# Kernel optimization log

Hardware: AMD Instinct MI355X
Metric: run time of the kernel (lower is better)

Reference implementation:

```python
import jax, jax.numpy as jnp
import numpy as np

B, NQ, NK, DQ, DK, H, DV = 4, 128, 1024, 256, 256, 256, 256
MASK_VAL = -1e6


def setup_inputs() -> dict:
    key = jax.random.key(0)
    ks = jax.random.split(key, 7)
    queries = jax.random.normal(ks[0], (B, NQ, DQ), dtype=jnp.float32)
    keys = jax.random.normal(ks[1], (B, NK, DK), dtype=jnp.float32)
    values = jax.random.normal(ks[2], (B, NK, DV), dtype=jnp.float32)
    # per-batch valid lengths in [1, NK]
    valid_lens = jax.random.randint(ks[3], (B,), 1, NK + 1, dtype=jnp.int64 if jax.config.read('jax_enable_x64') else jnp.int32)
    W_q = jax.random.normal(ks[4], (DQ, H), dtype=jnp.float32) * (1.0 / np.sqrt(DQ))
    W_k = jax.random.normal(ks[5], (DK, H), dtype=jnp.float32) * (1.0 / np.sqrt(DK))
    v_w = jax.random.normal(ks[6], (H,), dtype=jnp.float32) * (1.0 / np.sqrt(H))
    return {"queries": queries, "keys": keys, "values": values,
            "valid_lens": valid_lens, "W_q": W_q, "W_k": W_k, "v_w": v_w}


def reference(queries, keys, values, valid_lens, W_q, W_k, v_w):
    # Project queries and keys to the shared hidden space.
    q = jnp.einsum('bqd,dh->bqh', queries, W_q)          # (B, NQ, H)
    k = jnp.einsum('bkd,dh->bkh', keys, W_k)             # (B, NK, H)
    # Broadcast-add + tanh -> (B, NQ, NK, H), then contract with v to scores.
    features = jnp.tanh(q[:, :, None, :] + k[:, None, :, :])
    scores = jnp.einsum('bqkh,h->bqk', features, v_w)    # (B, NQ, NK)
    # Masked softmax over the key axis: positions >= valid_len get -1e6.
    nk = scores.shape[-1]
    mask = jnp.arange(nk)[None, None, :] < valid_lens[:, None, None]
    scores = jnp.where(mask, scores, MASK_VAL)
    attention_weights = jax.nn.softmax(scores, axis=-1)
    # Weighted sum of values (bmm).
    return jnp.einsum('bqk,bkv->bqv', attention_weights, values)
```

## Files before the change

### kernel.cpp

```cpp
#include <hip/hip_runtime.h>

#define B_   4
#define NQ_  128
#define NK_  1024
#define DD_  256
#define H_   256
#define DV_  256
#define QB   2

__device__ __forceinline__ float wave_sum(float v) {
  #pragma unroll
  for (int o = 32; o; o >>= 1) v += __shfl_xor(v, o);
  return v;
}
__device__ __forceinline__ float wave_max(float v) {
  #pragma unroll
  for (int o = 32; o; o >>= 1) v = fmaxf(v, __shfl_xor(v, o));
  return v;
}

template <bool TRANS>
__global__ __launch_bounds__(256) void proj_kernel(const float* __restrict__ A,
                                                   const float* __restrict__ W,
                                                   float* __restrict__ C) {
  __shared__ float As[16 * 68];
  __shared__ float Ws[16 * 68];
  const int tid  = threadIdx.x;
  const int row0 = blockIdx.x * 64;
  const int col0 = blockIdx.y * 64;
  const int ld_d = tid & 15, ld_r = tid >> 4;
  const int lw_n = tid & 63, lw_k = tid >> 6;
  const int tn = tid & 15, tm = tid >> 4;
  float acc[4][4] = {};
  for (int kt = 0; kt < DD_ / 16; ++kt) {
    const int k0 = kt * 16;
    #pragma unroll
    for (int p = 0; p < 4; ++p) {
      const int r = p * 16 + ld_r;
      As[ld_d * 68 + r] = A[(size_t)(row0 + r) * DD_ + (k0 + ld_d)];
    }
    #pragma unroll
    for (int p = 0; p < 4; ++p) {
      const int kk = p * 4 + lw_k;
      Ws[kk * 68 + lw_n] = W[(size_t)(k0 + kk) * H_ + (col0 + lw_n)];
    }
    __syncthreads();
    #pragma unroll
    for (int kk = 0; kk < 16; ++kk) {
      const float4 a = *(const float4*)&As[kk * 68 + tm * 4];
      const float4 w = *(const float4*)&Ws[kk * 68 + tn * 4];
      acc[0][0] = fmaf(a.x, w.x, acc[0][0]);
      acc[0][1] = fmaf(a.x, w.y, acc[0][1]);
      acc[0][2] = fmaf(a.x, w.z, acc[0][2]);
      acc[0][3] = fmaf(a.x, w.w, acc[0][3]);
      acc[1][0] = fmaf(a.y, w.x, acc[1][0]);
      acc[1][1] = fmaf(a.y, w.y, acc[1][1]);
      acc[1][2] = fmaf(a.y, w.z, acc[1][2]);
      acc[1][3] = fmaf(a.y, w.w, acc[1][3]);
      acc[2][0] = fmaf(a.z, w.x, acc[2][0]);
      acc[2][1] = fmaf(a.z, w.y, acc[2][1]);
      acc[2][2] = fmaf(a.z, w.z, acc[2][2]);
      acc[2][3] = fmaf(a.z, w.w, acc[2][3]);
      acc[3][0] = fmaf(a.w, w.x, acc[3][0]);
      acc[3][1] = fmaf(a.w, w.y, acc[3][1]);
      acc[3][2] = fmaf(a.w, w.z, acc[3][2]);
      acc[3][3] = fmaf(a.w, w.w, acc[3][3]);
    }
    __syncthreads();
  }
  if (!TRANS) {
    #pragma unroll
    for (int i = 0; i < 4; ++i) {
      float4 v = make_float4(acc[i][0], acc[i][1], acc[i][2], acc[i][3]);
      *(float4*)&C[(size_t)(row0 + tm * 4 + i) * H_ + (col0 + tn * 4)] = v;
    }
  } else {
    #pragma unroll
    for (int i = 0; i < 4; ++i) {
      const int row = row0 + tm * 4 + i;
      const int b = row >> 10;
      const int k = row & (NK_ - 1);
      #pragma unroll
      for (int j = 0; j < 4; ++j) {
        const int h = col0 + tn * 4 + j;
        C[((size_t)(b * H_ + h)) * NK_ + k] = acc[i][j];
      }
    }
  }
}

__global__ __launch_bounds__(512) void fused_attn_kernel(const float* __restrict__ qp,
                                                         const float* __restrict__ kpT,
                                                         const float* __restrict__ v_w,
                                                         const float* __restrict__ values,
                                                         const int* __restrict__ valid_lens,
                                                         float* __restrict__ out) {
  __shared__ float qs[QB][H_];
  __shared__ float w2s[H_];
  __shared__ float reds[4];
  __shared__ float s_lds[QB][NK_];
  __shared__ float redm[QB][4];
  __shared__ float redsum[QB][4];
  __shared__ float red[8][QB][DV_];

  const int tid = threadIdx.x;
  const int n = blockIdx.x;
  const int xcd = n & 7;
  const int b = xcd >> 1;
  const int idx = ((n >> 3) << 1) | (xcd & 1);

  int vl = valid_lens[b];
  vl = vl < 1 ? 1 : (vl > NK_ ? NK_ : vl);

  if (tid < H_) {
    const float vw = v_w[tid];
    w2s[tid] = 2.0f * vw;
    float s = wave_sum(vw);
    if ((tid & 63) == 0) reds[tid >> 6] = s;
  }
  {
    const int qi = tid >> 8, h = tid & 255;
    qs[qi][h] = qp[(size_t)(b * NQ_ + idx * QB + qi) * H_ + h];
  }
  __syncthreads();
  const float wsum = reds[0] + reds[1] + reds[2] + reds[3];

  const int k0 = tid * 2;
  const float C2 = 2.8853900817779268f;
  if (k0 < vl) {
    float a00 = 0.f, a01 = 0.f, a10 = 0.f, a11 = 0.f;
    const float* kp = kpT + (size_t)b * H_ * NK_ + k0;
    #pragma unroll 4
    for (int h = 0; h < H_; ++h) {
      const float2 kv = *(const float2*)(kp + (size_t)h * NK_);
      const float w2 = w2s[h];
      const float q0 = qs[0][h];
      const float q1 = qs[1][h];
      const float e00 = __builtin_amdgcn_exp2f((q0 + kv.x) * C2);
      const float e01 = __builtin_amdgcn_exp2f((q0 + kv.y) * C2);
      const float e10 = __builtin_amdgcn_exp2f((q1 + kv.x) * C2);
      const float e11 = __builtin_amdgcn_exp2f((q1 + kv.y) * C2);
      a00 = fmaf(w2, __builtin_amdgcn_rcpf(1.0f + e00), a00);
      a01 = fmaf(w2, __builtin_amdgcn_rcpf(1.0f + e01), a01);
      a10 = fmaf(w2, __builtin_amdgcn_rcpf(1.0f + e10), a10);
      a11 = fmaf(w2, __builtin_amdgcn_rcpf(1.0f + e11), a11);
    }
    *(float2*)&s_lds[0][k0] = make_float2(wsum - a00, wsum - a01);
    *(float2*)&s_lds[1][k0] = make_float2(wsum - a10, wsum - a11);
  }
  __syncthreads();

  const int qi = tid >> 8;
  const int kk0 = (tid & 255) * 4;
  const float4 s4 = *(const float4*)&s_lds[qi][kk0];
  const float NEG = -3.0e38f;
  float m = NEG;
  m = fmaxf(m, (kk0 + 0 < vl) ? s4.x : NEG);
  m = fmaxf(m, (kk0 + 1 < vl) ? s4.y : NEG);
  m = fmaxf(m, (kk0 + 2 < vl) ? s4.z : NEG);
  m = fmaxf(m, (kk0 + 3 < vl) ? s4.w : NEG);
  m = wave_max(m);
  if ((tid & 63) == 0) redm[qi][(tid >> 6) & 3] = m;
  __syncthreads();
  const float M = fmaxf(fmaxf(redm[qi][0], redm[qi][1]), fmaxf(redm[qi][2], redm[qi][3]));
  const float CE = 1.4426950408889634f;
  const float p0 = (kk0 + 0 < vl) ? __builtin_amdgcn_exp2f((s4.x - M) * CE) : 0.0f;
  const float p1 = (kk0 + 1 < vl) ? __builtin_amdgcn_exp2f((s4.y - M) * CE) : 0.0f;
  const float p2 = (kk0 + 2 < vl) ? __builtin_amdgcn_exp2f((s4.z - M) * CE) : 0.0f;
  const float p3 = (kk0 + 3 < vl) ? __builtin_amdgcn_exp2f((s4.w - M) * CE) : 0.0f;
  float psum = wave_sum(p0 + p1 + p2 + p3);
  if ((tid & 63) == 0) redsum[qi][(tid >> 6) & 3] = psum;
  __syncthreads();
  const float S = redsum[qi][0] + redsum[qi][1] + redsum[qi][2] + redsum[qi][3];
  const float inv = 1.0f / S;
  *(float4*)&s_lds[qi][kk0] = make_float4(p0 * inv, p1 * inv, p2 * inv, p3 * inv);
  __syncthreads();

  const int w = tid >> 6;
  const int lane = tid & 63;
  const int d0 = lane * 4;
  float4 pa0 = make_float4(0.f, 0.f, 0.f, 0.f);
  float4 pa1 = make_float4(0.f, 0.f, 0.f, 0.f);
  const int kbeg = w * (NK_ / 8);
  const int kend = (kbeg + NK_ / 8) < vl ? (kbeg + NK_ / 8) : vl;
  const float* vb = values + (size_t)b * NK_ * DV_ + d0;
  #pragma unroll 4
  for (int k = kbeg; k < kend; ++k) {
    const float4 v4 = *(const float4*)(vb + (size_t)k * DV_);
    const float w0 = s_lds[0][k];
    const float w1 = s_lds[1][k];
    pa0.x = fmaf(w0, v4.x, pa0.x);
    pa0.y = fmaf(w0, v4.y, pa0.y);
    pa0.z = fmaf(w0, v4.z, pa0.z);
    pa0.w = fmaf(w0, v4.w, pa0.w);
    pa1.x = fmaf(w1, v4.x, pa1.x);
    pa1.y = fmaf(w1, v4.y, pa1.y);
    pa1.z = fmaf(w1, v4.z, pa1.z);
    pa1.w = fmaf(w1, v4.w, pa1.w);
  }
  *(float4*)&red[w][0][d0] = pa0;
  *(float4*)&red[w][1][d0] = pa1;
  __syncthreads();

  const int oqi = tid >> 8;
  const int d = tid & 255;
  float s = 0.f;
  #pragma unroll
  for (int ww = 0; ww < 8; ++ww) s += red[ww][oqi][d];
  out[(size_t)(b * NQ_ + idx * QB + oqi) * DV_ + d] = s;
}

extern "C" void kernel_launch(void* const* d_in, const int* in_sizes, int n_in,
                              void* d_out, int out_size, void* d_ws, size_t ws_size,
                              hipStream_t stream) {
  const float* queries = (const float*)d_in[0];
  const float* keys    = (const float*)d_in[1];
  const float* values  = (const float*)d_in[2];
  const int*   vlens   = (const int*)d_in[3];
  const float* W_q     = (const float*)d_in[4];
  const float* W_k     = (const float*)d_in[5];
  const float* v_w     = (const float*)d_in[6];
  float* out = (float*)d_out;

  float* qp  = (float*)d_ws;
  float* kpT = qp + (size_t)B_ * NQ_ * H_;

  proj_kernel<false><<<dim3((B_ * NQ_) / 64, H_ / 64), 256, 0, stream>>>(queries, W_q, qp);
  proj_kernel<true ><<<dim3((B_ * NK_) / 64, H_ / 64), 256, 0, stream>>>(keys, W_k, kpT);
  fused_attn_kernel<<<(B_ * NQ_) / QB, 512, 0, stream>>>(qp, kpT, v_w, values, vlens, out);
}
```

Before: 150.1 us.

## Merge Q/K projections, prefetch tiles, coalesce kT store, split H across thread groups

Merges the query and key projection GEMMs into a single launch. Each K-tile's global loads are prefetched into registers, and the transposed key output is staged through LDS so it is written with coalesced float4 stores instead of scattered scalar ones. In the attention kernel, each thread now covers four keys over half of H, with the two halves summed afterwards, and q is pre-scaled so the tanh argument takes a single FMA. These changes aim to cut launch overhead, uncoalesced writes and ALU work in the tanh-score loop, at the cost of extra LDS and higher register pressure.

```diff
diff --git a/kernel.cpp b/kernel.cpp
--- a/kernel.cpp
+++ b/kernel.cpp
@@ -6,7 +6,6 @@
 #define DD_  256
 #define H_   256
 #define DV_  256
-#define QB   2
 
 __device__ __forceinline__ float wave_sum(float v) {
   #pragma unroll
@@ -19,32 +18,45 @@
   return v;
 }
 
-template <bool TRANS>
-__global__ __launch_bounds__(256) void proj_kernel(const float* __restrict__ A,
-                                                   const float* __restrict__ W,
-                                                   float* __restrict__ C) {
+__global__ __launch_bounds__(256) void proj_merged_kernel(
+    const float* __restrict__ queries, const float* __restrict__ keys,
+    const float* __restrict__ W_q, const float* __restrict__ W_k,
+    float* __restrict__ qp, float* __restrict__ kpT) {
   __shared__ float As[16 * 68];
   __shared__ float Ws[16 * 68];
+  __shared__ float Ts[64 * 68];
   const int tid  = threadIdx.x;
   const int row0 = blockIdx.x * 64;
   const int col0 = blockIdx.y * 64;
+  const bool isQ = row0 < 512;
+  const float* A = isQ ? queries + (size_t)row0 * DD_
+                       : keys + (size_t)(row0 - 512) * DD_;
+  const float* W = isQ ? W_q : W_k;
   const int ld_d = tid & 15, ld_r = tid >> 4;
   const int lw_n = tid & 63, lw_k = tid >> 6;
   const int tn = tid & 15, tm = tid >> 4;
+
+  float aP[4], wP[4];
+  #pragma unroll
+  for (int p = 0; p < 4; ++p) aP[p] = A[(size_t)(p * 16 + ld_r) * DD_ + ld_d];
+  #pragma unroll
+  for (int p = 0; p < 4; ++p) wP[p] = W[(size_t)(p * 4 + lw_k) * H_ + col0 + lw_n];
+
   float acc[4][4] = {};
-  for (int kt = 0; kt < DD_ / 16; ++kt) {
-    const int k0 = kt * 16;
-    #pragma unroll
-    for (int p = 0; p < 4; ++p) {
-      const int r = p * 16 + ld_r;
-      As[ld_d * 68 + r] = A[(size_t)(row0 + r) * DD_ + (k0 + ld_d)];
-    }
-    #pragma unroll
-    for (int p = 0; p < 4; ++p) {
-      const int kk = p * 4 + lw_k;
-      Ws[kk * 68 + lw_n] = W[(size_t)(k0 + kk) * H_ + (col0 + lw_n)];
-    }
+  for (int kt = 0; kt < 16; ++kt) {
     __syncthreads();
+    #pragma unroll
+    for (int p = 0; p < 4; ++p) As[ld_d * 68 + p * 16 + ld_r] = aP[p];
+    #pragma unroll
+    for (int p = 0; p < 4; ++p) Ws[(p * 4 + lw_k) * 68 + lw_n] = wP[p];
+    __syncthreads();
+    if (kt < 15) {
+      const int k0 = (kt + 1) * 16;
+      #pragma unroll
+      for (int p = 0; p < 4; ++p) aP[p] = A[(size_t)(p * 16 + ld_r) * DD_ + k0 + ld_d];
+      #pragma unroll
+      for (int p = 0; p < 4; ++p) wP[p] = W[(size_t)(k0 + p * 4 + lw_k) * H_ + col0 + lw_n];
+    }
     #pragma unroll
     for (int kk = 0; kk < 16; ++kk) {
       const float4 a = *(const float4*)&As[kk * 68 + tm * 4];
@@ -66,114 +78,133 @@
       acc[3][2] = fmaf(a.w, w.z, acc[3][2]);
       acc[3][3] = fmaf(a.w, w.w, acc[3][3]);
     }
+  }
+
+  if (isQ) {
+    #pragma unroll
+    for (int i = 0; i < 4; ++i) {
+      *(float4*)&qp[(size_t)(row0 + tm * 4 + i) * H_ + col0 + tn * 4] =
+          make_float4(acc[i][0], acc[i][1], acc[i][2], acc[i][3]);
+    }
+  } else {
+    #pragma unroll
+    for (int i = 0; i < 4; ++i)
+      #pragma unroll
+      for (int j = 0; j < 4; ++j)
+        Ts[(tn * 4 + j) * 68 + tm * 4 + i] = acc[i][j];
     __syncthreads();
-  }
-  if (!TRANS) {
-    #pragma unroll
-    for (int i = 0; i < 4; ++i) {
-      float4 v = make_float4(acc[i][0], acc[i][1], acc[i][2], acc[i][3]);
-      *(float4*)&C[(size_t)(row0 + tm * 4 + i) * H_ + (col0 + tn * 4)] = v;
-    }
-  } else {
-    #pragma unroll
-    for (int i = 0; i < 4; ++i) {
-      const int row = row0 + tm * 4 + i;
-      const int b = row >> 10;
-      const int k = row & (NK_ - 1);
-      #pragma unroll
-      for (int j = 0; j < 4; ++j) {
-        const int h = col0 + tn * 4 + j;
-        C[((size_t)(b * H_ + h)) * NK_ + k] = acc[i][j];
-      }
-    }
-  }
-}
-
-__global__ __launch_bounds__(512) void fused_attn_kernel(const float* __restrict__ qp,
-                                                         const float* __restrict__ kpT,
-                                                         const float* __restrict__ v_w,
-                                                         const float* __restrict__ values,
-                                                         const int* __restrict__ valid_lens,
-                                                         float* __restrict__ out) {
-  __shared__ float qs[QB][H_];
+    const int keyrow = row0 - 512;
+    const int b = keyrow >> 10;
+    const int kbase = keyrow & (NK_ - 1);
+    const int hh = tid >> 2;
+    const int kg = (tid & 3) * 16;
+    float* dst = kpT + ((size_t)(b * H_ + col0 + hh)) * NK_ + kbase + kg;
+    #pragma unroll
+    for (int p = 0; p < 4; ++p)
+      *(float4*)&dst[p * 4] = *(const float4*)&Ts[hh * 68 + kg + p * 4];
+  }
+}
+
+__global__ __launch_bounds__(512) void fused_attn_kernel(
+    const float* __restrict__ qp, const float* __restrict__ kpT,
+    const float* __restrict__ v_w, const float* __restrict__ values,
+    const int* __restrict__ valid_lens, float* __restrict__ out) {
+  __shared__ float2 qs2[H_];
   __shared__ float w2s[H_];
   __shared__ float reds[4];
-  __shared__ float s_lds[QB][NK_];
-  __shared__ float redm[QB][4];
-  __shared__ float redsum[QB][4];
-  __shared__ float red[8][QB][DV_];
+  __shared__ float s_half[2][2][NK_];
+  __shared__ float redm[2][4];
+  __shared__ float redsum[2][4];
+  __shared__ float red[8][2][DV_];
 
   const int tid = threadIdx.x;
   const int n = blockIdx.x;
   const int xcd = n & 7;
   const int b = xcd >> 1;
   const int idx = ((n >> 3) << 1) | (xcd & 1);
+  const int qrow = b * NQ_ + idx * 2;
 
   int vl = valid_lens[b];
   vl = vl < 1 ? 1 : (vl > NK_ ? NK_ : vl);
 
+  const float C2 = 2.8853900817779268f;
   if (tid < H_) {
     const float vw = v_w[tid];
     w2s[tid] = 2.0f * vw;
+    const float q0 = qp[(size_t)qrow * H_ + tid];
+    const float q1 = qp[(size_t)(qrow + 1) * H_ + tid];
+    qs2[tid] = make_float2(q0 * C2, q1 * C2);
     float s = wave_sum(vw);
     if ((tid & 63) == 0) reds[tid >> 6] = s;
   }
-  {
-    const int qi = tid >> 8, h = tid & 255;
-    qs[qi][h] = qp[(size_t)(b * NQ_ + idx * QB + qi) * H_ + h];
-  }
   __syncthreads();
   const float wsum = reds[0] + reds[1] + reds[2] + reds[3];
 
-  const int k0 = tid * 2;
-  const float C2 = 2.8853900817779268f;
+  const int g = tid >> 8;
+  const int t = tid & 255;
+  const int k0 = t * 4;
   if (k0 < vl) {
-    float a00 = 0.f, a01 = 0.f, a10 = 0.f, a11 = 0.f;
-    const float* kp = kpT + (size_t)b * H_ * NK_ + k0;
-    #pragma unroll 4
-    for (int h = 0; h < H_; ++h) {
-      const float2 kv = *(const float2*)(kp + (size_t)h * NK_);
-      const float w2 = w2s[h];
-      const float q0 = qs[0][h];
-      const float q1 = qs[1][h];
-      const float e00 = __builtin_amdgcn_exp2f((q0 + kv.x) * C2);
-      const float e01 = __builtin_amdgcn_exp2f((q0 + kv.y) * C2);
-      const float e10 = __builtin_amdgcn_exp2f((q1 + kv.x) * C2);
-      const float e11 = __builtin_amdgcn_exp2f((q1 + kv.y) * C2);
-      a00 = fmaf(w2, __builtin_amdgcn_rcpf(1.0f + e00), a00);
-      a01 = fmaf(w2, __builtin_amdgcn_rcpf(1.0f + e01), a01);
-      a10 = fmaf(w2, __builtin_amdgcn_rcpf(1.0f + e10), a10);
-      a11 = fmaf(w2, __builtin_amdgcn_rcpf(1.0f + e11), a11);
-    }
-    *(float2*)&s_lds[0][k0] = make_float2(wsum - a00, wsum - a01);
-    *(float2*)&s_lds[1][k0] = make_float2(wsum - a10, wsum - a11);
+    float a0x = 0.f, a0y = 0.f, a0z = 0.f, a0w = 0.f;
+    float a1x = 0.f, a1y = 0.f, a1z = 0.f, a1w = 0.f;
+    const float* kp = kpT + (size_t)b * H_ * NK_ + (size_t)(g * 128) * NK_ + k0;
+    #pragma unroll 2
+    for (int h = 0; h < 128; ++h) {
+      const float4 kv = *(const float4*)(kp + (size_t)h * NK_);
+      const int hh = g * 128 + h;
+      const float w2 = w2s[hh];
+      const float2 q2 = qs2[hh];
+      const float e0x = __builtin_amdgcn_exp2f(fmaf(kv.x, C2, q2.x));
+      const float e0y = __builtin_amdgcn_exp2f(fmaf(kv.y, C2, q2.x));
+      const float e0z = __builtin_amdgcn_exp2f(fmaf(kv.z, C2, q2.x));
+      const float e0w = __builtin_amdgcn_exp2f(fmaf(kv.w, C2, q2.x));
+      const float e1x = __builtin_amdgcn_exp2f(fmaf(kv.x, C2, q2.y));
+      const float e1y = __builtin_amdgcn_exp2f(fmaf(kv.y, C2, q2.y));
+      const float e1z = __builtin_amdgcn_exp2f(fmaf(kv.z, C2, q2.y));
+      const float e1w = __builtin_amdgcn_exp2f(fmaf(kv.w, C2, q2.y));
+      a0x = fmaf(w2, __builtin_amdgcn_rcpf(1.0f + e0x), a0x);
+      a0y = fmaf(w2, __builtin_amdgcn_rcpf(1.0f + e0y), a0y);
+      a0z = fmaf(w2, __builtin_amdgcn_rcpf(1.0f + e0z), a0z);
+      a0w = fmaf(w2, __builtin_amdgcn_rcpf(1.0f + e0w), a0w);
+      a1x = fmaf(w2, __builtin_amdgcn_rcpf(1.0f + e1x), a1x);
+      a1y = fmaf(w2, __builtin_amdgcn_rcpf(1.0f + e1y), a1y);
+      a1z = fmaf(w2, __builtin_amdgcn_rcpf(1.0f + e1z), a1z);
+      a1w = fmaf(w2, __builtin_amdgcn_rcpf(1.0f + e1w), a1w);
+    }
+    *(float4*)&s_half[g][0][k0] = make_float4(a0x, a0y, a0z, a0w);
+    *(float4*)&s_half[g][1][k0] = make_float4(a1x, a1y, a1z, a1w);
   }
   __syncthreads();
 
   const int qi = tid >> 8;
-  const int kk0 = (tid & 255) * 4;
-  const float4 s4 = *(const float4*)&s_lds[qi][kk0];
+  const int k4 = (tid & 255) * 4;
+  const float4 pA = *(const float4*)&s_half[0][qi][k4];
+  const float4 pB = *(const float4*)&s_half[1][qi][k4];
+  const float s0 = wsum - (pA.x + pB.x);
+  const float s1 = wsum - (pA.y + pB.y);
+  const float s2 = wsum - (pA.z + pB.z);
+  const float s3 = wsum - (pA.w + pB.w);
   const float NEG = -3.0e38f;
   float m = NEG;
-  m = fmaxf(m, (kk0 + 0 < vl) ? s4.x : NEG);
-  m = fmaxf(m, (kk0 + 1 < vl) ? s4.y : NEG);
-  m = fmaxf(m, (kk0 + 2 < vl) ? s4.z : NEG);
-  m = fmaxf(m, (kk0 + 3 < vl) ? s4.w : NEG);
+  m = fmaxf(m, (k4 + 0 < vl) ? s0 : NEG);
+  m = fmaxf(m, (k4 + 1 < vl) ? s1 : NEG);
+  m = fmaxf(m, (k4 + 2 < vl) ? s2 : NEG);
+  m = fmaxf(m, (k4 + 3 < vl) ? s3 : NEG);
   m = wave_max(m);
   if ((tid & 63) == 0) redm[qi][(tid >> 6) & 3] = m;
   __syncthreads();
-  const float M = fmaxf(fmaxf(redm[qi][0], redm[qi][1]), fmaxf(redm[qi][2], redm[qi][3]));
+  const float M = fmaxf(fmaxf(redm[qi][0], redm[qi][1]),
+                        fmaxf(redm[qi][2], redm[qi][3]));
   const float CE = 1.4426950408889634f;
-  const float p0 = (kk0 + 0 < vl) ? __builtin_amdgcn_exp2f((s4.x - M) * CE) : 0.0f;
-  const float p1 = (kk0 + 1 < vl) ? __builtin_amdgcn_exp2f((s4.y - M) * CE) : 0.0f;
-  const float p2 = (kk0 + 2 < vl) ? __builtin_amdgcn_exp2f((s4.z - M) * CE) : 0.0f;
-  const float p3 = (kk0 + 3 < vl) ? __builtin_amdgcn_exp2f((s4.w - M) * CE) : 0.0f;
+  const float p0 = (k4 + 0 < vl) ? __builtin_amdgcn_exp2f((s0 - M) * CE) : 0.0f;
+  const float p1 = (k4 + 1 < vl) ? __builtin_amdgcn_exp2f((s1 - M) * CE) : 0.0f;
+  const float p2 = (k4 + 2 < vl) ? __builtin_amdgcn_exp2f((s2 - M) * CE) : 0.0f;
+  const float p3 = (k4 + 3 < vl) ? __builtin_amdgcn_exp2f((s3 - M) * CE) : 0.0f;
   float psum = wave_sum(p0 + p1 + p2 + p3);
   if ((tid & 63) == 0) redsum[qi][(tid >> 6) & 3] = psum;
   __syncthreads();
   const float S = redsum[qi][0] + redsum[qi][1] + redsum[qi][2] + redsum[qi][3];
   const float inv = 1.0f / S;
-  *(float4*)&s_lds[qi][kk0] = make_float4(p0 * inv, p1 * inv, p2 * inv, p3 * inv);
+  *(float4*)&s_half[0][qi][k4] = make_float4(p0 * inv, p1 * inv, p2 * inv, p3 * inv);
   __syncthreads();
 
   const int w = tid >> 6;
@@ -187,8 +218,8 @@
   #pragma unroll 4
   for (int k = kbeg; k < kend; ++k) {
     const float4 v4 = *(const float4*)(vb + (size_t)k * DV_);
-    const float w0 = s_lds[0][k];
-    const float w1 = s_lds[1][k];
+    const float w0 = s_half[0][0][k];
+    const float w1 = s_half[0][1][k];
     pa0.x = fmaf(w0, v4.x, pa0.x);
     pa0.y = fmaf(w0, v4.y, pa0.y);
     pa0.z = fmaf(w0, v4.z, pa0.z);
@@ -207,7 +238,7 @@
   float s = 0.f;
   #pragma unroll
   for (int ww = 0; ww < 8; ++ww) s += red[ww][oqi][d];
-  out[(size_t)(b * NQ_ + idx * QB + oqi) * DV_ + d] = s;
+  out[(size_t)(qrow + oqi) * DV_ + d] = s;
 }
 
 extern "C" void kernel_launch(void* const* d_in, const int* in_sizes, int n_in,
@@ -225,7 +256,7 @@
   float* qp  = (float*)d_ws;
   float* kpT = qp + (size_t)B_ * NQ_ * H_;
 
-  proj_kernel<false><<<dim3((B_ * NQ_) / 64, H_ / 64), 256, 0, stream>>>(queries, W_q, qp);
-  proj_kernel<true ><<<dim3((B_ * NK_) / 64, H_ / 64), 256, 0, stream>>>(keys, W_k, kpT);
-  fused_attn_kernel<<<(B_ * NQ_) / QB, 512, 0, stream>>>(qp, kpT, v_w, values, vlens, out);
-}
+  proj_merged_kernel<<<dim3((512 + B_ * NK_) / 64, H_ / 64), 256, 0, stream>>>(
+      queries, keys, W_q, W_k, qp, kpT);
+  fused_attn_kernel<<<(B_ * NQ_) / 2, 512, 0, stream>>>(qp, kpT, v_w, values, vlens, out);
+}
```

Result: faster. 132.1 us (-12.0%).
